# Performance work log

Hardware: AMD Instinct MI355X
Metric: run time of the kernel (lower is better)

The kernel has to match this reference:

```python
import jax, jax.numpy as jnp
import numpy as np
from jax import lax

NUM_STEPS = 32
NUM_CLASSES = 10
HIDDEN = 1024


def setup_inputs() -> dict:
    key = jax.random.key(0)
    ks = jax.random.split(key, 4)
    B, H, W, C = 8, 1024, 2048, 4
    x = jax.random.normal(ks[0], (B, H, W, C), dtype=jnp.float32)
    conv_w = jax.random.normal(ks[1], (C,), dtype=jnp.float32) * 0.5
    conv_b = jnp.zeros((1,), dtype=jnp.float32)
    w1 = jax.random.normal(ks[2], (HIDDEN, W), dtype=jnp.float32) * (1.0 / np.sqrt(W))
    b1 = jnp.zeros((HIDDEN,), dtype=jnp.float32)
    w2 = jax.random.normal(ks[3], (NUM_CLASSES, HIDDEN), dtype=jnp.float32) * (1.0 / np.sqrt(HIDDEN))
    b2 = jnp.zeros((NUM_CLASSES,), dtype=jnp.float32)
    beta1 = jnp.full((1,), 0.95, dtype=jnp.float32)
    thr1 = jnp.ones((1,), dtype=jnp.float32)
    beta2 = jnp.full((1,), 0.95, dtype=jnp.float32)
    thr2 = jnp.ones((1,), dtype=jnp.float32)
    return {"x": x, "conv_w": conv_w, "conv_b": conv_b, "w1": w1, "b1": b1,
            "beta1": beta1, "thr1": thr1, "w2": w2, "b2": b2,
            "beta2": beta2, "thr2": thr2}


def _leaky_scan(inp_t, beta, thr):
    # inp_t: [T, ...]; snntorch Leaky, reset_mechanism='subtract', reset_delay=False
    b = jnp.clip(beta, 0.0, 1.0)

    def step(mem, u):
        mem = b * mem + u
        spk = (mem > thr).astype(u.dtype)   # heaviside spike
        mem = mem - spk * thr               # subtract reset (no delay)
        return mem, spk

    mem0 = jnp.zeros(inp_t.shape[1:], dtype=inp_t.dtype)
    _, spks = lax.scan(step, mem0, inp_t)
    return spks  # [T, ...]


def reference(x, conv_w, conv_b, w1, b1, beta1, thr1, w2, b2, beta2, thr2):
    # x: [B, H, W, 4]; 1x1 conv over 4 antenna channels -> 1 channel
    xf = jnp.einsum('bhwc,c->bhw', x, conv_w) + conv_b[0]       # [B, H, W]
    B, H, W = xf.shape
    G = H // NUM_STEPS
    xr = xf.reshape(B, G, NUM_STEPS, W)                          # [B, G, T, 2048]
    h = jnp.einsum('bgtw,dw->bgtd', xr, w1) + b1                 # [B, G, T, D]
    spks1 = _leaky_scan(jnp.moveaxis(h, 2, 0), beta1, thr1)      # [T, B, G, D]
    s = spks1.sum(axis=0)                                        # [B, G, D]
    h2 = jnp.einsum('bgd,cd->bgc', s, w2) + b2                   # [B, G, C]
    spks2 = _leaky_scan(jnp.moveaxis(h2, 1, 0), beta2, thr2)     # [G, B, C]
    logits = spks2.sum(axis=0)                                   # [B, C]
    return jax.nn.softmax(logits, axis=1)
```

## Files before the change

### kernel.cpp

```cpp
#include <hip/hip_runtime.h>

#define TSTEPS 32
#define HID 1024
#define NCLS 10
#define BATCH 8
#define GGRP 32
#define MROWS 8192
#define GK 2048
#define GN 1024

typedef __attribute__((ext_vector_type(8))) short bf16x8;
typedef __attribute__((ext_vector_type(4))) float f32x4;

__device__ __forceinline__ unsigned short bf16_rne(float v) {
    unsigned u = __builtin_bit_cast(unsigned, v);
    return (unsigned short)((u + 0x7FFFu + ((u >> 16) & 1u)) >> 16);
}
__device__ __forceinline__ float bf16_f(unsigned short h) {
    unsigned u = (unsigned)h << 16;
    return __builtin_bit_cast(float, u);
}
__device__ __forceinline__ void gload16(const unsigned short* g, unsigned short* l) {
    __builtin_amdgcn_global_load_lds(
        (const __attribute__((address_space(1))) void*)g,
        (__attribute__((address_space(3))) void*)l, 16, 0, 0);
}


__global__ __launch_bounds__(256) void conv_pack_kernel(
    const float4* __restrict__ x, const float* __restrict__ cw,
    const float* __restrict__ cb,
    unsigned short* __restrict__ Ahi, unsigned short* __restrict__ Alo)
{
    const int rb = blockIdx.x >> 6;
    const int kb = blockIdx.x & 63;
    const float c0 = cw[0], c1 = cw[1], c2 = cw[2], c3 = cw[3], cbv = cb[0];
    const int tid = threadIdx.x;
#pragma unroll
    for (int cc = 0; cc < 2; ++cc) {
        int c = tid + cc * 256;
        int kc = c >> 7, row = c & 127;
        const float4* px = x + ((size_t)(rb * 128 + row) * 2048 + kb * 32 + kc * 8);
        bf16x8 h8, l8;
#pragma unroll
        for (int e = 0; e < 8; ++e) {
            float4 a = px[e];
            float v = a.x * c0 + a.y * c1 + a.z * c2 + a.w * c3 + cbv;
            unsigned short h = bf16_rne(v);
            h8[e] = (short)h;
            l8[e] = (short)bf16_rne(v - bf16_f(h));
        }
        size_t off = ((size_t)blockIdx.x * 512 + c) * 8;
        *(bf16x8*)(Ahi + off) = h8;
        *(bf16x8*)(Alo + off) = l8;
    }
}

__global__ __launch_bounds__(256) void wpack_kernel(
    const float* __restrict__ w, unsigned short* __restrict__ Bhi,
    unsigned short* __restrict__ Blo)
{
    const int kb = blockIdx.x & 63;
    const int cbk = blockIdx.x >> 6;
    const int tid = threadIdx.x;
#pragma unroll
    for (int cc = 0; cc < 2; ++cc) {
        int c = tid + cc * 256;
        int kc = c >> 7, row = c & 127;
        const float* pw = w + ((size_t)(cbk * 128 + row) * 2048 + kb * 32 + kc * 8);
        bf16x8 h8, l8;
#pragma unroll
        for (int e = 0; e < 8; ++e) {
            float v = pw[e];
            unsigned short h = bf16_rne(v);
            h8[e] = (short)h;
            l8[e] = (short)bf16_rne(v - bf16_f(h));
        }
        size_t off = ((size_t)blockIdx.x * 512 + c) * 8;
        *(bf16x8*)(Bhi + off) = h8;
        *(bf16x8*)(Blo + off) = l8;
    }
}

__global__ __launch_bounds__(256) void gemm_scan_kernel(
    const unsigned short* __restrict__ Ahi, const unsigned short* __restrict__ Alo,
    const unsigned short* __restrict__ Bhi, const unsigned short* __restrict__ Blo,
    const float* __restrict__ bias,
    const float* __restrict__ beta1, const float* __restrict__ thr1,
    float* __restrict__ S)
{
    __shared__ __align__(16) unsigned short smem[2][16384];

    const int tid = threadIdx.x;
    const int lane = tid & 63, wv = tid >> 6;
    const int wr = wv >> 1, wc = wv & 1;
    const int lm = lane & 15, lk = lane >> 4;
    const int rb = blockIdx.y;
    const int col0 = blockIdx.x * 128;

    const unsigned short* gAh = Ahi + (size_t)rb * (64 * 4096);
    const unsigned short* gAl = Alo + (size_t)rb * (64 * 4096);
    const unsigned short* gBh = Bhi + (size_t)blockIdx.x * (64 * 4096);
    const unsigned short* gBl = Blo + (size_t)blockIdx.x * (64 * 4096);

    f32x4 acc[4][4];
#pragma unroll
    for (int i = 0; i < 4; ++i)
#pragma unroll
        for (int j = 0; j < 4; ++j) acc[i][j] = (f32x4)0.f;

#define STAGE(buf, kb_)                                                          \
    {                                                                            \
        const size_t tb = (size_t)(kb_) * 4096;                                  \
        unsigned short* dst = &smem[buf][0];                                     \
        _Pragma("unroll")                                                        \
        for (int ii = 0; ii < 2; ++ii) {                                         \
            size_t so = tb + (size_t)(wv * 128 + ii * 64 + lane) * 8;            \
            int dl = (wv * 128 + ii * 64) * 8;                                   \
            gload16(gAh + so, dst + 0 + dl);                                     \
            gload16(gAl + so, dst + 4096 + dl);                                  \
            gload16(gBh + so, dst + 8192 + dl);                                  \
            gload16(gBl + so, dst + 12288 + dl);                                 \
        }                                                                        \
    }

    STAGE(0, 0);
    __syncthreads();

    int cur = 0;
    for (int kb = 0; kb < 64; ++kb) {
        if (kb < 63) STAGE(cur ^ 1, kb + 1);

        const unsigned short* bufp = &smem[cur][0];
        bf16x8 ah[4], al[4], bh[4], bl[4];
#pragma unroll
        for (int i = 0; i < 4; ++i) {
            int ca = lk * 128 + wr * 64 + i * 16 + lm;
            int cb2 = lk * 128 + wc * 64 + i * 16 + lm;
            ah[i] = *(const bf16x8*)(bufp + 0 + ca * 8);
            al[i] = *(const bf16x8*)(bufp + 4096 + ca * 8);
            bh[i] = *(const bf16x8*)(bufp + 8192 + cb2 * 8);
            bl[i] = *(const bf16x8*)(bufp + 12288 + cb2 * 8);
        }
#pragma unroll
        for (int i = 0; i < 4; ++i)
#pragma unroll
            for (int j = 0; j < 4; ++j) {
                acc[i][j] = __builtin_amdgcn_mfma_f32_16x16x32_bf16(ah[i], bh[j], acc[i][j], 0, 0, 0);
                acc[i][j] = __builtin_amdgcn_mfma_f32_16x16x32_bf16(ah[i], bl[j], acc[i][j], 0, 0, 0);
                acc[i][j] = __builtin_amdgcn_mfma_f32_16x16x32_bf16(al[i], bh[j], acc[i][j], 0, 0, 0);
            }
        __syncthreads();
        cur ^= 1;
    }

    float* sb = (float*)&smem[0][0];
    const float bclamp = fminf(fmaxf(beta1[0], 0.f), 1.f);
    const float th = thr1[0];
    const int sbg = tid >> 7;
    const int scol = tid & 127;
    const float bv = bias[col0 + scol];

#pragma unroll
    for (int band = 0; band < 2; ++band) {
        if (wr == band) {
#pragma unroll
            for (int i = 0; i < 4; ++i)
#pragma unroll
                for (int j = 0; j < 4; ++j)
#pragma unroll
                    for (int r = 0; r < 4; ++r)
                        sb[(i * 16 + lk * 4 + r) * 132 + wc * 64 + j * 16 + lm] = acc[i][j][r];
        }
        __syncthreads();
        float mem = 0.f, cnt = 0.f;
#pragma unroll
        for (int t = 0; t < TSTEPS; ++t) {
            float u = sb[(sbg * 32 + t) * 132 + scol] + bv;
            mem = bclamp * mem + u;
            float spk = mem > th ? 1.f : 0.f;
            mem -= spk * th;
            cnt += spk;
        }
        int bgg = ((rb * 128) >> 5) + band * 2 + sbg;
        S[(size_t)bgg * GN + col0 + scol] = cnt;
        __syncthreads();
    }
}

__global__ __launch_bounds__(256) void fc2_kernel(
    const float* __restrict__ s, const float* __restrict__ w2,
    const float* __restrict__ b2, float* __restrict__ h2)
{
    int bg  = blockIdx.x;
    int tid = threadIdx.x;
    const float* sp = s + (size_t)bg * HID;
    float part[NCLS];
#pragma unroll
    for (int c = 0; c < NCLS; ++c) part[c] = 0.f;
    for (int d = tid; d < HID; d += 256) {
        float sv = sp[d];
#pragma unroll
        for (int c = 0; c < NCLS; ++c) part[c] += sv * w2[c * HID + d];
    }
#pragma unroll
    for (int c = 0; c < NCLS; ++c)
        for (int off = 32; off > 0; off >>= 1)
            part[c] += __shfl_down(part[c], off, 64);
    __shared__ float red[NCLS][4];
    int wave = tid >> 6, lanei = tid & 63;
    if (lanei == 0)
#pragma unroll
        for (int c = 0; c < NCLS; ++c) red[c][wave] = part[c];
    __syncthreads();
    if (tid < NCLS) {
        float v = red[tid][0] + red[tid][1] + red[tid][2] + red[tid][3] + b2[tid];
        h2[bg * NCLS + tid] = v;
    }
}

__global__ __launch_bounds__(128) void scan2_kernel(
    const float* __restrict__ h2, const float* __restrict__ beta2,
    const float* __restrict__ thr2, float* __restrict__ out)
{
    __shared__ float logits[BATCH][NCLS];
    int t = threadIdx.x;
    if (t < BATCH * NCLS) {
        int b = t / NCLS, c = t % NCLS;
        float bb = fminf(fmaxf(beta2[0], 0.f), 1.f);
        float th = thr2[0];
        float mem = 0.f, lg = 0.f;
        for (int g = 0; g < GGRP; ++g) {
            float u = h2[(b * GGRP + g) * NCLS + c];
            mem = bb * mem + u;
            float spk = mem > th ? 1.f : 0.f;
            mem -= spk * th;
            lg += spk;
        }
        logits[b][c] = lg;
    }
    __syncthreads();
    if (t < BATCH) {
        float mx = -1e30f;
        for (int c = 0; c < NCLS; ++c) mx = fmaxf(mx, logits[t][c]);
        float e[NCLS];
        float sum = 0.f;
        for (int c = 0; c < NCLS; ++c) { e[c] = expf(logits[t][c] - mx); sum += e[c]; }
        for (int c = 0; c < NCLS; ++c) out[t * NCLS + c] = e[c] / sum;
    }
}

extern "C" void kernel_launch(void* const* d_in, const int* in_sizes, int n_in,
                              void* d_out, int out_size, void* d_ws, size_t ws_size,
                              hipStream_t stream)
{
    const float* x     = (const float*)d_in[0];
    const float* cw    = (const float*)d_in[1];
    const float* cb    = (const float*)d_in[2];
    const float* w1    = (const float*)d_in[3];
    const float* b1    = (const float*)d_in[4];
    const float* beta1 = (const float*)d_in[5];
    const float* thr1  = (const float*)d_in[6];
    const float* w2    = (const float*)d_in[7];
    const float* b2    = (const float*)d_in[8];
    const float* beta2 = (const float*)d_in[9];
    const float* thr2  = (const float*)d_in[10];
    float* out = (float*)d_out;

    unsigned short* ahi = (unsigned short*)d_ws;
    unsigned short* alo = ahi + (size_t)MROWS * GK;
    unsigned short* bhi = alo + (size_t)MROWS * GK;
    unsigned short* blo = bhi + (size_t)GN * GK;
    float* s  = (float*)(blo + (size_t)GN * GK);
    float* h2 = s + (size_t)BATCH * GGRP * HID;

    conv_pack_kernel<<<4096, 256, 0, stream>>>((const float4*)x, cw, cb, ahi, alo);
    wpack_kernel    <<<512, 256, 0, stream>>>(w1, bhi, blo);
    gemm_scan_kernel<<<dim3(8, 64), 256, 0, stream>>>(ahi, alo, bhi, blo, b1, beta1, thr1, s);
    fc2_kernel      <<<256, 256, 0, stream>>>(s, w2, b2, h2);
    scan2_kernel    <<<1, 128, 0, stream>>>(h2, beta2, thr2, out);
}
```

Baseline: 173.7 us.

## Switch split-bf16 GEMM to 32x32x16 MFMA with matching pack layout

Replaces the 16x16x32 bf16 MFMA tiling (4x4 tiles per wave) with 32x32x16 MFMA (2x2 tiles of 16 accumulators), rearranging the packed A/B layout in the conv and weight pack kernels so each lane's fragment is a contiguous 16-byte LDS read. The epilogue scatter is updated to the 32x32 accumulator layout. The larger MFMA shape needs fewer instructions and LDS reads per FLOP, but register pressure and the ordering of accumulation change.

New measurement: 179.7 us. +3.5%, slower.

```diff
diff --git a/kernel.cpp b/kernel.cpp
--- a/kernel.cpp
+++ b/kernel.cpp
@@ -10,7 +10,7 @@
 #define GN 1024
 
 typedef __attribute__((ext_vector_type(8))) short bf16x8;
-typedef __attribute__((ext_vector_type(4))) float f32x4;
+typedef __attribute__((ext_vector_type(16))) float f32x16;
 
 __device__ __forceinline__ unsigned short bf16_rne(float v) {
     unsigned u = __builtin_bit_cast(unsigned, v);
@@ -39,8 +39,10 @@
 #pragma unroll
     for (int cc = 0; cc < 2; ++cc) {
         int c = tid + cc * 256;
-        int kc = c >> 7, row = c & 127;
-        const float4* px = x + ((size_t)(rb * 128 + row) * 2048 + kb * 32 + kc * 8);
+        int u = c >> 6, w = c & 63;
+        int row = (u >> 1) * 32 + (w & 31);
+        int k0  = (u & 1) * 16 + (w >> 5) * 8;
+        const float4* px = x + ((size_t)(rb * 128 + row) * 2048 + kb * 32 + k0);
         bf16x8 h8, l8;
 #pragma unroll
         for (int e = 0; e < 8; ++e) {
@@ -57,7 +59,7 @@
 }
 
 __global__ __launch_bounds__(256) void wpack_kernel(
-    const float* __restrict__ w, unsigned short* __restrict__ Bhi,
+    const float* __restrict__ wsrc, unsigned short* __restrict__ Bhi,
     unsigned short* __restrict__ Blo)
 {
     const int kb = blockIdx.x & 63;
@@ -66,8 +68,10 @@
 #pragma unroll
     for (int cc = 0; cc < 2; ++cc) {
         int c = tid + cc * 256;
-        int kc = c >> 7, row = c & 127;
-        const float* pw = w + ((size_t)(cbk * 128 + row) * 2048 + kb * 32 + kc * 8);
+        int u = c >> 6, w = c & 63;
+        int row = (u >> 1) * 32 + (w & 31);
+        int k0  = (u & 1) * 16 + (w >> 5) * 8;
+        const float* pw = wsrc + ((size_t)(cbk * 128 + row) * 2048 + kb * 32 + k0);
         bf16x8 h8, l8;
 #pragma unroll
         for (int e = 0; e < 8; ++e) {
@@ -94,7 +98,6 @@
     const int tid = threadIdx.x;
     const int lane = tid & 63, wv = tid >> 6;
     const int wr = wv >> 1, wc = wv & 1;
-    const int lm = lane & 15, lk = lane >> 4;
     const int rb = blockIdx.y;
     const int col0 = blockIdx.x * 128;
 
@@ -103,11 +106,11 @@
     const unsigned short* gBh = Bhi + (size_t)blockIdx.x * (64 * 4096);
     const unsigned short* gBl = Blo + (size_t)blockIdx.x * (64 * 4096);
 
-    f32x4 acc[4][4];
-#pragma unroll
-    for (int i = 0; i < 4; ++i)
-#pragma unroll
-        for (int j = 0; j < 4; ++j) acc[i][j] = (f32x4)0.f;
+    f32x16 acc[2][2];
+#pragma unroll
+    for (int i = 0; i < 2; ++i)
+#pragma unroll
+        for (int j = 0; j < 2; ++j) acc[i][j] = (f32x16)0.f;
 
 #define STAGE(buf, kb_)                                                          \
     {                                                                            \
@@ -127,29 +130,43 @@
     STAGE(0, 0);
     __syncthreads();
 
+    const int fo = ((lane & 31) + 32 * (lane >> 5)) * 8;
+
     int cur = 0;
     for (int kb = 0; kb < 64; ++kb) {
         if (kb < 63) STAGE(cur ^ 1, kb + 1);
 
         const unsigned short* bufp = &smem[cur][0];
-        bf16x8 ah[4], al[4], bh[4], bl[4];
-#pragma unroll
-        for (int i = 0; i < 4; ++i) {
-            int ca = lk * 128 + wr * 64 + i * 16 + lm;
-            int cb2 = lk * 128 + wc * 64 + i * 16 + lm;
-            ah[i] = *(const bf16x8*)(bufp + 0 + ca * 8);
-            al[i] = *(const bf16x8*)(bufp + 4096 + ca * 8);
-            bh[i] = *(const bf16x8*)(bufp + 8192 + cb2 * 8);
-            bl[i] = *(const bf16x8*)(bufp + 12288 + cb2 * 8);
-        }
-#pragma unroll
-        for (int i = 0; i < 4; ++i)
-#pragma unroll
-            for (int j = 0; j < 4; ++j) {
-                acc[i][j] = __builtin_amdgcn_mfma_f32_16x16x32_bf16(ah[i], bh[j], acc[i][j], 0, 0, 0);
-                acc[i][j] = __builtin_amdgcn_mfma_f32_16x16x32_bf16(ah[i], bl[j], acc[i][j], 0, 0, 0);
-                acc[i][j] = __builtin_amdgcn_mfma_f32_16x16x32_bf16(al[i], bh[j], acc[i][j], 0, 0, 0);
+        bf16x8 ah[2][2], al[2][2], bh[2][2], bl[2][2];
+#pragma unroll
+        for (int i = 0; i < 2; ++i)
+#pragma unroll
+            for (int kh = 0; kh < 2; ++kh) {
+                int ua = (((wr * 2 + i) * 2 + kh) << 9) + fo;
+                int ub = (((wc * 2 + i) * 2 + kh) << 9) + fo;
+                ah[i][kh] = *(const bf16x8*)(bufp + 0 + ua);
+                al[i][kh] = *(const bf16x8*)(bufp + 4096 + ua);
+                bh[i][kh] = *(const bf16x8*)(bufp + 8192 + ub);
+                bl[i][kh] = *(const bf16x8*)(bufp + 12288 + ub);
             }
+#pragma unroll
+        for (int kh = 0; kh < 2; ++kh) {
+#pragma unroll
+            for (int i = 0; i < 2; ++i)
+#pragma unroll
+                for (int j = 0; j < 2; ++j)
+                    acc[i][j] = __builtin_amdgcn_mfma_f32_32x32x16_bf16(ah[i][kh], bh[j][kh], acc[i][j], 0, 0, 0);
+#pragma unroll
+            for (int i = 0; i < 2; ++i)
+#pragma unroll
+                for (int j = 0; j < 2; ++j)
+                    acc[i][j] = __builtin_amdgcn_mfma_f32_32x32x16_bf16(ah[i][kh], bl[j][kh], acc[i][j], 0, 0, 0);
+#pragma unroll
+            for (int i = 0; i < 2; ++i)
+#pragma unroll
+                for (int j = 0; j < 2; ++j)
+                    acc[i][j] = __builtin_amdgcn_mfma_f32_32x32x16_bf16(al[i][kh], bh[j][kh], acc[i][j], 0, 0, 0);
+        }
         __syncthreads();
         cur ^= 1;
     }
@@ -165,12 +182,15 @@
     for (int band = 0; band < 2; ++band) {
         if (wr == band) {
 #pragma unroll
-            for (int i = 0; i < 4; ++i)
-#pragma unroll
-                for (int j = 0; j < 4; ++j)
-#pragma unroll
-                    for (int r = 0; r < 4; ++r)
-                        sb[(i * 16 + lk * 4 + r) * 132 + wc * 64 + j * 16 + lm] = acc[i][j][r];
+            for (int i = 0; i < 2; ++i)
+#pragma unroll
+                for (int j = 0; j < 2; ++j)
+#pragma unroll
+                    for (int r = 0; r < 16; ++r) {
+                        int lr = i * 32 + (r & 3) + 8 * (r >> 2) + 4 * (lane >> 5);
+                        int lc = wc * 64 + j * 32 + (lane & 31);
+                        sb[lr * 132 + lc] = acc[i][j][r];
+                    }
         }
         __syncthreads();
         float mem = 0.f, cnt = 0.f;
```
